# Kernel tuning notes

Measured on AMD Instinct MI355X. Metric: run time of the kernel, lower is better.

## Reference

```python
import jax, jax.numpy as jnp
import numpy as np

IMAGE_W = 256
IMAGE_H = 256
EPS = 1e-07
SIGMA2 = 2.0 * 0.1 ** 2  # 2 * sigma^2 with sigma = 0.1


def _norm(x, eps=EPS):
    # min/max over stroke dim (axis=1), per batch
    mn = x.min(axis=1, keepdims=True)
    mx = x.max(axis=1, keepdims=True)
    return (x - mn) / (mx - mn + eps)


def setup_inputs() -> dict:
    key = jax.random.key(0)
    k1, k2 = jax.random.split(key)
    brushes = jax.random.uniform(k1, (16, 64, 2), dtype=jnp.float32)
    patches = jax.random.normal(k2, (16, 64, 3, 32, 32), dtype=jnp.float32)
    return {"brushes": brushes, "patches": patches}


def reference(brushes, patches):
    B, N, _ = brushes.shape
    C, ph, pw = patches.shape[2], patches.shape[3], patches.shape[4]
    w, h = IMAGE_W, IMAGE_H
    pad = ph // 2  # 'half_patch'

    gx = _norm(brushes[:, :, 0]) * w  # [B, N]
    gy = _norm(brushes[:, :, 1]) * h

    # grid coordinates (original builds 2D index arrays whose columns are identical;
    # a 1D arange is the equivalent efficient form)
    a = jnp.arange(w + 2 * pad, dtype=jnp.float32) - pad  # [w+2p]
    b = jnp.arange(h + 2 * pad, dtype=jnp.float32) - pad  # [h+2p]
    widths = jnp.arange(1, pw + 1, dtype=jnp.float32)
    heights = jnp.arange(1, ph + 1, dtype=jnp.float32)

    ux = gx[:, :, None] + (widths - pw / 2 - 0.5)   # [B, N, pw]
    uy = gy[:, :, None] + (heights - pw / 2 - 0.4)  # [B, N, ph] (pw/2 offset as in source)

    # separable Gaussian filter banks, normalized over the padded spatial axis
    Fx = jnp.exp(-((a[None, None, :, None] - ux[:, :, None, :]) ** 2) / SIGMA2)  # [B,N,w+2p,pw]
    Fx = Fx / (Fx.sum(axis=2, keepdims=True) + EPS)
    Fx = Fx[:, :, pad:-pad]  # [B, N, w, pw]

    Fy = jnp.exp(-((b[None, None, :, None] - uy[:, :, None, :]) ** 2) / SIGMA2)  # [B,N,h+2p,ph]
    Fy = Fy / (Fy.sum(axis=2, keepdims=True) + EPS)
    Fy = Fy[:, :, pad:-pad]  # [B, N, h, ph]

    # separable splat: out[b,c,y,x] = mean_n sum_{p,q} Fy[b,n,y,p] Fx[b,n,x,q] patches[b,n,c,p,q]
    t = jnp.einsum('bnxq,bncpq->bncxp', Fx, patches)  # [B,N,C,w,ph]
    out = jnp.einsum('bncxp,bnyp->bcyx', t, Fy) / N   # mean over strokes -> [B,C,h,w]
    return out
```

## Files before the change

kernel.cpp:

```cpp
#include <hip/hip_runtime.h>
#include <type_traits>

#define IMG_W 256
#define IMG_H 256
#define EPSN 1e-7f
#define NS 50.0f
#define NB 16
#define NN 64
#define NC 3
#define PH 32
#define PW 32
#define NWG 2048

__global__ __launch_bounds__(192)
void fused_kernel(const float* __restrict__ brushes,
                  const float* __restrict__ patches,
                  float* __restrict__ out) {
    __shared__ float2 sG[NN];
    __shared__ int    sN[NN];
    __shared__ int    sPb[NN];
    __shared__ float  sSx[NN];
    __shared__ float4 sWx[NN];
    __shared__ float4 sEyC[NN];
    __shared__ float4 sEy31[NN];
    __shared__ int    sCnt;

    int blk = blockIdx.x;
    blk = (blk & 7) * (NWG >> 3) + (blk >> 3);

    const int b    = blk >> 7;
    const int t7   = blk & 127;
    const int ty0  = (t7 >> 3) * 16;
    const int tx0  = (t7 & 7) * 32;
    const int tid  = threadIdx.x;
    const int cc   = tid >> 6;
    const int lane = tid & 63;
    const int ysub = lane >> 3;
    const int xgrp = lane & 7;
    const int ax0  = tx0 + xgrp * 4;
    const int ay0  = ty0 + ysub * 2;

    if (tid < 64) {
        float2 v = ((const float2*)brushes)[b * NN + tid];
        float mnx = v.x, mxx = v.x, mny = v.y, mxy = v.y;
        #pragma unroll
        for (int off = 32; off > 0; off >>= 1) {
            mnx = fminf(mnx, __shfl_xor(mnx, off));
            mxx = fmaxf(mxx, __shfl_xor(mxx, off));
            mny = fminf(mny, __shfl_xor(mny, off));
            mxy = fmaxf(mxy, __shfl_xor(mxy, off));
        }
        float gx = (v.x - mnx) / (mxx - mnx + EPSN) * (float)IMG_W;
        float gy = (v.y - mny) / (mxy - mny + EPSN) * (float)IMG_H;
        int ix0 = (int)floorf(gx) - 17;
        int iy0 = (int)floorf(gy) - 17;
        bool ov = (ix0 <= tx0 + 31) && (ix0 + 35 >= tx0) &&
                  (iy0 <= ty0 + 15) && (iy0 + 35 >= ty0);
        unsigned long long mask = __ballot(ov);
        if (ov) {
            int pos = __popcll(mask & ((1ull << tid) - 1));
            sN[pos] = tid;
            sG[pos] = make_float2(gx, gy);

            float px  = 15.5f - gx;
            float phx = px - floorf(px);
            float Ex[4];
            #pragma unroll
            for (int k = 0; k < 4; ++k) {
                float d = phx + (float)(1 - k);
                Ex[k] = __expf(-NS * d * d);
            }
            float Sx  = ((Ex[0] + Ex[1]) + (Ex[2] + Ex[3]));
            float Dxc = 1.f / (Sx + EPSN);
            sSx[pos] = Sx;
            sWx[pos] = make_float4(Ex[0] * Dxc, Ex[1] * Dxc,
                                   Ex[2] * Dxc, Ex[3] * Dxc);

            float zy0 = (float)ty0 - gy + 15.4f;
            float fz  = floorf(zy0);
            sPb[pos]  = (int)fz - 1;
            float psy = zy0 - fz;
            float Ey[4];
            #pragma unroll
            for (int k = 0; k < 4; ++k) {
                float d = psy + (float)(1 - k);
                Ey[k] = __expf(-NS * d * d);
            }
            float Sy  = ((Ey[0] + Ey[1]) + (Ey[2] + Ey[3]));
            float DyC = (1.f / (Sy + EPSN)) * (1.0f / (float)NN);
            float Dy31 = DyC;
            if (gy > 254.9f) {
                float cy31 = gy + 15.6f;
                float dc   = 272.f - cy31;
                float c272 = __expf(-NS * dc * dc);
                Dy31 = (1.f / (Sy - c272 + EPSN)) * (1.0f / (float)NN);
            }
            sEyC[pos]  = make_float4(Ey[0] * DyC,  Ey[1] * DyC,
                                     Ey[2] * DyC,  Ey[3] * DyC);
            sEy31[pos] = make_float4(Ey[0] * Dy31, Ey[1] * Dy31,
                                     Ey[2] * Dy31, Ey[3] * Dy31);
        }
        if (tid == 0) sCnt = (int)__popcll(mask);
    }
    __syncthreads();
    const int cnt = sCnt;

    float acc[2][4];
    #pragma unroll
    for (int j = 0; j < 2; ++j)
        #pragma unroll
        for (int o = 0; o < 4; ++o) acc[j][o] = 0.f;

    const float* Pcb = patches + (size_t)b * NN * (NC * PH * PW) + cc * (PH * PW);

    for (int i = 0; i < cnt; ++i) {
        const float2 g = sG[i];
        const int    n = sN[i];
        const float* Pc = Pcb + (size_t)n * (NC * PH * PW);

        const float zx0 = (float)ax0 - g.x + 15.5f;
        const int   q00 = (int)floorf(zx0) - 1;

        if (q00 >= -6 && q00 <= 31) {
            const float4 W4 = sWx[i];
            const float  W[4] = {W4.x, W4.y, W4.z, W4.w};
            const int    pb = sPb[i];

            const float4 eC = sEyC[i];
            const float4 e3 = sEy31[i];
            const float eyC[4]  = {eC.x, eC.y, eC.z, eC.w};
            const float ey31[4] = {e3.x, e3.y, e3.z, e3.w};
            float wyA[4], wyB[4];
            #pragma unroll
            for (int k = 0; k < 4; ++k) {
                int rA = pb + 2 * ysub + k;
                int rB = rA + 1;
                wyA[k] = ((unsigned)rA < 32u) ? ((rA == 31) ? ey31[k] : eyC[k]) : 0.f;
                wyB[k] = ((unsigned)rB < 32u) ? ((rB == 31) ? ey31[k] : eyC[k]) : 0.f;
            }

            const int qg = ((q00 + 8) & ~3) - 8;
            const int M  = (q00 + 8) & 3;
            const int s1 = qg + 4, s2 = qg + 8;
            const float m0 = (qg >= 0 && qg <= 28) ? 1.f : 0.f;
            const float m1 = (s1 >= 0 && s1 <= 28) ? 1.f : 0.f;
            const float m2 = (s2 >= 0 && s2 <= 28) ? 1.f : 0.f;
            const int c0 = min(max(qg, 0), 28);
            const int c1 = min(max(s1, 0), 28);
            const int c2 = min(max(s2, 0), 28);

            auto rows = [&](auto Mc) {
                constexpr int Mv = Mc.value;
                #pragma unroll
                for (int rr = 0; rr < 5; ++rr) {
                    int src = min(max(pb + 2 * ysub + rr, 0), 31);
                    const float* rp = Pc + (src << 5);
                    float4 A  = *(const float4*)(rp + c0);
                    float4 Bv = *(const float4*)(rp + c1);
                    float cx0 = 0.f, cx1 = 0.f, cx2 = 0.f, cx3 = 0.f;
                    if constexpr (Mv >= 2) {
                        float4 Cv = *(const float4*)(rp + c2);
                        cx0 = Cv.x * m2; cx1 = Cv.y * m2;
                        cx2 = Cv.z * m2; cx3 = Cv.w * m2;
                    }
                    float pv[12] = {A.x * m0, A.y * m0, A.z * m0, A.w * m0,
                                    Bv.x * m1, Bv.y * m1, Bv.z * m1, Bv.w * m1,
                                    cx0, cx1, cx2, cx3};
                    float tr[4];
                    #pragma unroll
                    for (int o = 0; o < 4; ++o)
                        tr[o] = W[0] * pv[Mv + o]     + W[1] * pv[Mv + o + 1]
                              + W[2] * pv[Mv + o + 2] + W[3] * pv[Mv + o + 3];
                    if (rr < 4) {
                        #pragma unroll
                        for (int o = 0; o < 4; ++o) acc[0][o] += wyA[rr] * tr[o];
                    }
                    if (rr >= 1) {
                        #pragma unroll
                        for (int o = 0; o < 4; ++o) acc[1][o] += wyB[rr - 1] * tr[o];
                    }
                }
            };
            switch (M) {
                case 0: rows(std::integral_constant<int, 0>{}); break;
                case 1: rows(std::integral_constant<int, 1>{}); break;
                case 2: rows(std::integral_constant<int, 2>{}); break;
                default: rows(std::integral_constant<int, 3>{}); break;
            }

            if (g.x > 255.0f) {
                float Sx_  = sSx[i];
                float Dxc_ = 1.f / (Sx_ + EPSN);
                float cx31 = g.x + 15.5f;
                float dc   = 272.f - cx31;
                float c272 = __expf(-NS * dc * dc);
                float dD   = 1.f / (Sx_ - c272 + EPSN) - Dxc_;
                float e31[4];
                #pragma unroll
                for (int o = 0; o < 4; ++o) {
                    float d = zx0 + (float)o - 31.f;
                    e31[o] = __expf(-NS * d * d) * dD;
                }
                #pragma unroll
                for (int rr = 0; rr < 5; ++rr) {
                    int src = min(max(pb + 2 * ysub + rr, 0), 31);
                    float p31 = Pc[(src << 5) + 31];
                    float ta[4];
                    #pragma unroll
                    for (int o = 0; o < 4; ++o) ta[o] = e31[o] * p31;
                    if (rr < 4) {
                        #pragma unroll
                        for (int o = 0; o < 4; ++o) acc[0][o] += wyA[rr] * ta[o];
                    }
                    if (rr >= 1) {
                        #pragma unroll
                        for (int o = 0; o < 4; ++o) acc[1][o] += wyB[rr - 1] * ta[o];
                    }
                }
            }
        }
    }

    #pragma unroll
    for (int j = 0; j < 2; ++j) {
        float* o = out + (((size_t)b * NC + cc) * IMG_H + ay0 + j) * IMG_W + ax0;
        *(float4*)o = make_float4(acc[j][0], acc[j][1], acc[j][2], acc[j][3]);
    }
}

extern "C" void kernel_launch(void* const* d_in, const int* in_sizes, int n_in,
                              void* d_out, int out_size, void* d_ws, size_t ws_size,
                              hipStream_t stream) {
    const float* brushes = (const float*)d_in[0];
    const float* patches = (const float*)d_in[1];
    float* out = (float*)d_out;

    fused_kernel<<<NWG, 192, 0, stream>>>(brushes, patches, out);
}
```

Measured before the change: 24.08 us.

## Precompute per-stroke metadata in a separate kernel and bit-reverse tile order

Moves the per-batch min/max normalization and the Gaussian weight computation into a small pre-kernel that writes per-stroke metadata to workspace. The main kernel then only loads this metadata instead of recomputing it in each of 2048 workgroups. It also permutes the tile index within each batch by bit-reversal to change the order in which tiles are scheduled. The cost is an extra kernel launch and a serial dependency between the two kernels. The row-offset rewrite (floor(15.4-gy)+ty0 in place of floor(ty0-gy+15.4)) may differ slightly in floating point.

```diff
diff --git a/kernel.cpp b/kernel.cpp
--- a/kernel.cpp
+++ b/kernel.cpp
@@ -12,8 +12,73 @@
 #define PW 32
 #define NWG 2048
 
+#define MS ((size_t)NB * NN)
+
+__global__ __launch_bounds__(64)
+void meta_kernel(const float* __restrict__ brushes,
+                 float2* __restrict__ mG,
+                 float4* __restrict__ mWx,
+                 float4* __restrict__ mEyC,
+                 float4* __restrict__ mEy31,
+                 float2* __restrict__ mMisc) {
+    const int b = blockIdx.x;
+    const int n = threadIdx.x;
+    float2 v = ((const float2*)brushes)[b * NN + n];
+    float mnx = v.x, mxx = v.x, mny = v.y, mxy = v.y;
+    #pragma unroll
+    for (int off = 32; off > 0; off >>= 1) {
+        mnx = fminf(mnx, __shfl_xor(mnx, off));
+        mxx = fmaxf(mxx, __shfl_xor(mxx, off));
+        mny = fminf(mny, __shfl_xor(mny, off));
+        mxy = fmaxf(mxy, __shfl_xor(mxy, off));
+    }
+    float gx = (v.x - mnx) / (mxx - mnx + EPSN) * (float)IMG_W;
+    float gy = (v.y - mny) / (mxy - mny + EPSN) * (float)IMG_H;
+    const int s = b * NN + n;
+    mG[s] = make_float2(gx, gy);
+
+    float px  = 15.5f - gx;
+    float phx = px - floorf(px);
+    float Ex[4];
+    #pragma unroll
+    for (int k = 0; k < 4; ++k) {
+        float d = phx + (float)(1 - k);
+        Ex[k] = __expf(-NS * d * d);
+    }
+    float Sx  = ((Ex[0] + Ex[1]) + (Ex[2] + Ex[3]));
+    float Dxc = 1.f / (Sx + EPSN);
+    mWx[s] = make_float4(Ex[0] * Dxc, Ex[1] * Dxc, Ex[2] * Dxc, Ex[3] * Dxc);
+
+    float py  = 15.4f - gy;
+    float fy  = floorf(py);
+    int   pbG = (int)fy - 1;
+    float psy = py - fy;
+    float Ey[4];
+    #pragma unroll
+    for (int k = 0; k < 4; ++k) {
+        float d = psy + (float)(1 - k);
+        Ey[k] = __expf(-NS * d * d);
+    }
+    float Sy  = ((Ey[0] + Ey[1]) + (Ey[2] + Ey[3]));
+    float DyC = (1.f / (Sy + EPSN)) * (1.0f / (float)NN);
+    float Dy31 = DyC;
+    if (gy > 254.9f) {
+        float cy31 = gy + 15.6f;
+        float dc   = 272.f - cy31;
+        float c272 = __expf(-NS * dc * dc);
+        Dy31 = (1.f / (Sy - c272 + EPSN)) * (1.0f / (float)NN);
+    }
+    mEyC[s]  = make_float4(Ey[0] * DyC,  Ey[1] * DyC,  Ey[2] * DyC,  Ey[3] * DyC);
+    mEy31[s] = make_float4(Ey[0] * Dy31, Ey[1] * Dy31, Ey[2] * Dy31, Ey[3] * Dy31);
+    mMisc[s] = make_float2(Sx, (float)pbG);
+}
+
 __global__ __launch_bounds__(192)
-void fused_kernel(const float* __restrict__ brushes,
+void fused_kernel(const float2* __restrict__ mG,
+                  const float4* __restrict__ mWx,
+                  const float4* __restrict__ mEyC,
+                  const float4* __restrict__ mEy31,
+                  const float2* __restrict__ mMisc,
                   const float* __restrict__ patches,
                   float* __restrict__ out) {
     __shared__ float2 sG[NN];
@@ -27,9 +92,12 @@
 
     int blk = blockIdx.x;
     blk = (blk & 7) * (NWG >> 3) + (blk >> 3);
-
-    const int b    = blk >> 7;
-    const int t7   = blk & 127;
+    const int b  = blk >> 7;
+    unsigned r = blk & 127;
+    r = ((r & 0x55u) << 1) | ((r >> 1) & 0x55u);
+    r = ((r & 0x33u) << 2) | ((r >> 2) & 0x33u);
+    r = ((r & 0x0Fu) << 4) | ((r >> 4) & 0x0Fu);
+    const int t7 = (int)(r >> 1);
     const int ty0  = (t7 >> 3) * 16;
     const int tx0  = (t7 & 7) * 32;
     const int tid  = threadIdx.x;
@@ -41,64 +109,23 @@
     const int ay0  = ty0 + ysub * 2;
 
     if (tid < 64) {
-        float2 v = ((const float2*)brushes)[b * NN + tid];
-        float mnx = v.x, mxx = v.x, mny = v.y, mxy = v.y;
-        #pragma unroll
-        for (int off = 32; off > 0; off >>= 1) {
-            mnx = fminf(mnx, __shfl_xor(mnx, off));
-            mxx = fmaxf(mxx, __shfl_xor(mxx, off));
-            mny = fminf(mny, __shfl_xor(mny, off));
-            mxy = fmaxf(mxy, __shfl_xor(mxy, off));
-        }
-        float gx = (v.x - mnx) / (mxx - mnx + EPSN) * (float)IMG_W;
-        float gy = (v.y - mny) / (mxy - mny + EPSN) * (float)IMG_H;
-        int ix0 = (int)floorf(gx) - 17;
-        int iy0 = (int)floorf(gy) - 17;
+        const int s = b * NN + tid;
+        float2 g = mG[s];
+        int ix0 = (int)floorf(g.x) - 17;
+        int iy0 = (int)floorf(g.y) - 17;
         bool ov = (ix0 <= tx0 + 31) && (ix0 + 35 >= tx0) &&
                   (iy0 <= ty0 + 15) && (iy0 + 35 >= ty0);
         unsigned long long mask = __ballot(ov);
         if (ov) {
             int pos = __popcll(mask & ((1ull << tid) - 1));
-            sN[pos] = tid;
-            sG[pos] = make_float2(gx, gy);
-
-            float px  = 15.5f - gx;
-            float phx = px - floorf(px);
-            float Ex[4];
-            #pragma unroll
-            for (int k = 0; k < 4; ++k) {
-                float d = phx + (float)(1 - k);
-                Ex[k] = __expf(-NS * d * d);
-            }
-            float Sx  = ((Ex[0] + Ex[1]) + (Ex[2] + Ex[3]));
-            float Dxc = 1.f / (Sx + EPSN);
-            sSx[pos] = Sx;
-            sWx[pos] = make_float4(Ex[0] * Dxc, Ex[1] * Dxc,
-                                   Ex[2] * Dxc, Ex[3] * Dxc);
-
-            float zy0 = (float)ty0 - gy + 15.4f;
-            float fz  = floorf(zy0);
-            sPb[pos]  = (int)fz - 1;
-            float psy = zy0 - fz;
-            float Ey[4];
-            #pragma unroll
-            for (int k = 0; k < 4; ++k) {
-                float d = psy + (float)(1 - k);
-                Ey[k] = __expf(-NS * d * d);
-            }
-            float Sy  = ((Ey[0] + Ey[1]) + (Ey[2] + Ey[3]));
-            float DyC = (1.f / (Sy + EPSN)) * (1.0f / (float)NN);
-            float Dy31 = DyC;
-            if (gy > 254.9f) {
-                float cy31 = gy + 15.6f;
-                float dc   = 272.f - cy31;
-                float c272 = __expf(-NS * dc * dc);
-                Dy31 = (1.f / (Sy - c272 + EPSN)) * (1.0f / (float)NN);
-            }
-            sEyC[pos]  = make_float4(Ey[0] * DyC,  Ey[1] * DyC,
-                                     Ey[2] * DyC,  Ey[3] * DyC);
-            sEy31[pos] = make_float4(Ey[0] * Dy31, Ey[1] * Dy31,
-                                     Ey[2] * Dy31, Ey[3] * Dy31);
+            sN[pos]    = tid;
+            sG[pos]    = g;
+            sWx[pos]   = mWx[s];
+            sEyC[pos]  = mEyC[s];
+            sEy31[pos] = mEy31[s];
+            float2 ms  = mMisc[s];
+            sSx[pos]   = ms.x;
+            sPb[pos]   = (int)ms.y + ty0;
         }
         if (tid == 0) sCnt = (int)__popcll(mask);
     }
@@ -235,5 +262,14 @@
     const float* patches = (const float*)d_in[1];
     float* out = (float*)d_out;
 
-    fused_kernel<<<NWG, 192, 0, stream>>>(brushes, patches, out);
+    char* ws = (char*)d_ws;
+    float2* mG    = (float2*)(ws);
+    float4* mWx   = (float4*)(ws + 8192);
+    float4* mEyC  = (float4*)(ws + 8192 + 16384);
+    float4* mEy31 = (float4*)(ws + 8192 + 32768);
+    float2* mMisc = (float2*)(ws + 8192 + 49152);
+
+    meta_kernel<<<NB, 64, 0, stream>>>(brushes, mG, mWx, mEyC, mEy31, mMisc);
+    fused_kernel<<<NWG, 192, 0, stream>>>(mG, mWx, mEyC, mEy31, mMisc,
+                                          patches, out);
 }
```

Measured after the change: 27.89 us. +15.8%, slower.
